# Kernel optimization log

Measured on AMD Instinct MI355X. Metric: run time of the kernel, lower is better.

The kernel has to match this reference:

```python
import jax, jax.numpy as jnp
import numpy as np

MARGIN = 0.1
SEMIHARD = True


def setup_inputs() -> dict:
    key = jax.random.key(0)
    k1, k2 = jax.random.split(key)
    N, D = 512, 128
    embeddings = jax.random.normal(k1, (N, D), dtype=jnp.float32)
    labels = jax.random.randint(k2, (N,), 0, 64, dtype=jnp.int64)
    return {"embeddings": embeddings, "labels": labels}


def _triplet_mask(labels):
    # mask[a, p, n] True iff a,p,n distinct, labels[a]==labels[p], labels[a]!=labels[n]
    n = labels.shape[0]
    ine = ~jnp.eye(n, dtype=bool)                       # [N, N] i != j
    distinct = ine[:, :, None] & ine[:, None, :] & ine[None, :, :]
    leq = labels[None, :] == labels[:, None]            # [N, N] label equality
    valid = leq[:, :, None] & ~leq[:, None, :]
    return distinct & valid


def reference(embeddings, labels):
    # L2-normalize rows, cosine similarity matrix
    norms = jnp.linalg.norm(embeddings, ord=2, axis=1, keepdims=True)
    e = embeddings / norms
    all_sim = e @ e.T                                   # [N, N]
    mask = _triplet_mask(labels).astype(all_sim.dtype)  # [N, N, N]
    # loss[a,p,n] = relu(-sim[a,p] + sim[a,n] + margin) * mask
    anc_pos = all_sim[:, :, None]                       # [N, N, 1]
    anc_neg = all_sim[:, None, :]                       # [N, 1, N]
    loss = jax.nn.relu(anc_neg - anc_pos + MARGIN) * mask
    if SEMIHARD:
        num_active = jnp.sum((loss > 1e-16).astype(loss.dtype))
        return jnp.sum(loss) / (num_active + 1e-16)
    else:
        return jnp.sum(loss) / jnp.sum(mask)
```

## Files before the change

kernel.cpp:

```cpp
#include <hip/hip_runtime.h>
#include <math.h>

#define MARGIN 0.1f
#define NN 512
#define DD 128
#define NT 512
#define AB 2
#define GROUPS (NT / 4)
#define NTILES (NN / GROUPS)
#define NBLK (NN / AB)
#define MAXPOS 256

__global__ __launch_bounds__(NT) void triplet_partial_kernel(
        const float* __restrict__ emb, const int* __restrict__ labels,
        double* __restrict__ part_sum, int* __restrict__ part_cnt) {
    __shared__ int   lab[NN];
    __shared__ __align__(16) float ea[AB][DD];
    __shared__ float simr[AB][NN];
    __shared__ int   pos[AB][MAXPOS];
    __shared__ int   npos[AB];
    __shared__ double red_s[NT / 64];
    __shared__ int    red_c[NT / 64];

    const int b  = blockIdx.x;
    const int t  = threadIdx.x;
    const int a0 = b * AB;
    const int g  = t >> 2;
    const int ks = t & 3;

    lab[t] = labels[t];
    if (t < AB * DD) {
        ea[t >> 7][t & 127] = emb[(size_t)(a0 + (t >> 7)) * DD + (t & 127)];
    }
    if (t < AB) npos[t] = 0;
    __syncthreads();

    const float4* __restrict__ emb4 = reinterpret_cast<const float4*>(emb);
    const float4* ea4 = reinterpret_cast<const float4*>(&ea[0][0]);

    float4 w0[8], w1[8];
    #pragma unroll
    for (int i2 = 0; i2 < 8; ++i2) {
        w0[i2] = ea4[i2 * 4 + ks];
        w1[i2] = ea4[32 + i2 * 4 + ks];
    }

    float nsq0 = 0.f, nsq1 = 0.f;
    #pragma unroll
    for (int i2 = 0; i2 < 8; ++i2) {
        nsq0 += w0[i2].x * w0[i2].x + w0[i2].y * w0[i2].y
              + w0[i2].z * w0[i2].z + w0[i2].w * w0[i2].w;
        nsq1 += w1[i2].x * w1[i2].x + w1[i2].y * w1[i2].y
              + w1[i2].z * w1[i2].z + w1[i2].w * w1[i2].w;
    }
    nsq0 += __shfl_xor(nsq0, 1, 64); nsq0 += __shfl_xor(nsq0, 2, 64);
    nsq1 += __shfl_xor(nsq1, 1, 64); nsq1 += __shfl_xor(nsq1, 2, 64);
    const float inva0 = 1.0f / sqrtf(nsq0);
    const float inva1 = 1.0f / sqrtf(nsq1);

    #pragma unroll 2
    for (int tl = 0; tl < NTILES; ++tl) {
        const int r = tl * GROUPS + g;
        float4 v[8];
        #pragma unroll
        for (int i2 = 0; i2 < 8; ++i2)
            v[i2] = emb4[(size_t)r * 32 + i2 * 4 + ks];

        float d0a = 0.f, d0b = 0.f, d1a = 0.f, d1b = 0.f, na = 0.f, nb = 0.f;
        #pragma unroll
        for (int i2 = 0; i2 < 8; i2 += 2) {
            d0a += v[i2].x * w0[i2].x + v[i2].y * w0[i2].y
                 + v[i2].z * w0[i2].z + v[i2].w * w0[i2].w;
            d1a += v[i2].x * w1[i2].x + v[i2].y * w1[i2].y
                 + v[i2].z * w1[i2].z + v[i2].w * w1[i2].w;
            na  += v[i2].x * v[i2].x + v[i2].y * v[i2].y
                 + v[i2].z * v[i2].z + v[i2].w * v[i2].w;
            const int j2 = i2 + 1;
            d0b += v[j2].x * w0[j2].x + v[j2].y * w0[j2].y
                 + v[j2].z * w0[j2].z + v[j2].w * w0[j2].w;
            d1b += v[j2].x * w1[j2].x + v[j2].y * w1[j2].y
                 + v[j2].z * w1[j2].z + v[j2].w * w1[j2].w;
            nb  += v[j2].x * v[j2].x + v[j2].y * v[j2].y
                 + v[j2].z * v[j2].z + v[j2].w * v[j2].w;
        }
        float d0 = d0a + d0b, d1 = d1a + d1b, nsq = na + nb;

        d0  += __shfl_xor(d0, 1, 64);  d0  += __shfl_xor(d0, 2, 64);
        d1  += __shfl_xor(d1, 1, 64);  d1  += __shfl_xor(d1, 2, 64);
        nsq += __shfl_xor(nsq, 1, 64); nsq += __shfl_xor(nsq, 2, 64);
        if (ks == 0) {
            const float rn = 1.0f / sqrtf(nsq);
            simr[0][r] = d0 * inva0 * rn;
            simr[1][r] = d1 * inva1 * rn;
        }
    }
    __syncthreads();

    {
        const int j = t;
        #pragma unroll
        for (int ai = 0; ai < AB; ++ai) {
            if (j != a0 + ai && lab[j] == lab[a0 + ai]) {
                int idx = atomicAdd(&npos[ai], 1);
                if (idx < MAXPOS) pos[ai][idx] = j;
            }
        }
    }
    __syncthreads();

    const int   myLab = lab[t];
    const float sn0   = simr[0][t];
    const float sn1   = simr[1][t];
    double lsum = 0.0;
    int    lcnt = 0;
    {
        const int la = lab[a0];
        if (myLab != la) {
            const int np = min(npos[0], MAXPOS);
            for (int pi = 0; pi < np; ++pi) {
                const float sap = simr[0][pos[0][pi]];
                const float d = sn0 - sap + MARGIN;
                if (d > 0.f)    lsum += (double)d;
                if (d > 1e-16f) lcnt += 1;
            }
        }
    }
    {
        const int la = lab[a0 + 1];
        if (myLab != la) {
            const int np = min(npos[1], MAXPOS);
            for (int pi = 0; pi < np; ++pi) {
                const float sap = simr[1][pos[1][pi]];
                const float d = sn1 - sap + MARGIN;
                if (d > 0.f)    lsum += (double)d;
                if (d > 1e-16f) lcnt += 1;
            }
        }
    }

    for (int off = 32; off > 0; off >>= 1) {
        lsum += __shfl_down(lsum, off, 64);
        lcnt += __shfl_down(lcnt, off, 64);
    }
    const int wid = t >> 6, lane = t & 63;
    if (lane == 0) { red_s[wid] = lsum; red_c[wid] = lcnt; }
    __syncthreads();
    if (t == 0) {
        double s = 0.0; int c = 0;
        for (int w = 0; w < NT / 64; ++w) { s += red_s[w]; c += red_c[w]; }
        part_sum[b] = s;
        part_cnt[b] = c;
    }
}

__global__ __launch_bounds__(NBLK) void finalize_kernel(
        const double* __restrict__ part_sum, const int* __restrict__ part_cnt,
        float* __restrict__ out) {
    __shared__ double rs[NBLK / 64];
    __shared__ int    rc[NBLK / 64];
    const int t = threadIdx.x;
    double s = part_sum[t];
    int    c = part_cnt[t];
    for (int off = 32; off > 0; off >>= 1) {
        s += __shfl_down(s, off, 64);
        c += __shfl_down(c, off, 64);
    }
    const int wid = t >> 6, lane = t & 63;
    if (lane == 0) { rs[wid] = s; rc[wid] = c; }
    __syncthreads();
    if (t == 0) {
        double S = 0.0; int C = 0;
        for (int w = 0; w < NBLK / 64; ++w) { S += rs[w]; C += rc[w]; }
        out[0] = (float)(S / ((double)C + 1e-16));
    }
}

extern "C" void kernel_launch(void* const* d_in, const int* in_sizes, int n_in,
                              void* d_out, int out_size, void* d_ws, size_t ws_size,
                              hipStream_t stream) {
    const float* emb  = (const float*)d_in[0];
    const int* labels = (const int*)d_in[1];

    double* part_sum = (double*)d_ws;
    int*    part_cnt = (int*)((char*)d_ws + NBLK * sizeof(double));
    float*  out      = (float*)d_out;

    triplet_partial_kernel<<<NBLK, NT, 0, stream>>>(emb, labels, part_sum, part_cnt);
    finalize_kernel<<<1, NBLK, 0, stream>>>(part_sum, part_cnt, out);
}
```

Baseline: 63.29 us.

## Fuse final reduction into main kernel via last-block atomic counters

After: 66.49 us. 1.05x slower.

```diff
diff --git a/kernel.cpp b/kernel.cpp
--- a/kernel.cpp
+++ b/kernel.cpp
@@ -6,19 +6,23 @@
 #define DD 128
 #define NT 512
 #define AB 2
+#define NBLK (NN / AB)
 #define GROUPS (NT / 4)
 #define NTILES (NN / GROUPS)
-#define NBLK (NN / AB)
 #define MAXPOS 256
-
-__global__ __launch_bounds__(NT) void triplet_partial_kernel(
+#define NSUB 8
+#define GSZ (NBLK / NSUB)
+
+__global__ __launch_bounds__(NT) void triplet_fused_kernel(
         const float* __restrict__ emb, const int* __restrict__ labels,
-        double* __restrict__ part_sum, int* __restrict__ part_cnt) {
+        double* __restrict__ part_sum, int* __restrict__ part_cnt,
+        unsigned* __restrict__ sub_cnt, unsigned* __restrict__ super_cnt,
+        const unsigned* __restrict__ probe, float* __restrict__ out) {
     __shared__ int   lab[NN];
-    __shared__ __align__(16) float ea[AB][DD];
     __shared__ float simr[AB][NN];
     __shared__ int   pos[AB][MAXPOS];
     __shared__ int   npos[AB];
+    __shared__ int   islast;
     __shared__ double red_s[NT / 64];
     __shared__ int    red_c[NT / 64];
 
@@ -29,20 +33,15 @@
     const int ks = t & 3;
 
     lab[t] = labels[t];
-    if (t < AB * DD) {
-        ea[t >> 7][t & 127] = emb[(size_t)(a0 + (t >> 7)) * DD + (t & 127)];
-    }
     if (t < AB) npos[t] = 0;
-    __syncthreads();
 
     const float4* __restrict__ emb4 = reinterpret_cast<const float4*>(emb);
-    const float4* ea4 = reinterpret_cast<const float4*>(&ea[0][0]);
 
     float4 w0[8], w1[8];
     #pragma unroll
     for (int i2 = 0; i2 < 8; ++i2) {
-        w0[i2] = ea4[i2 * 4 + ks];
-        w1[i2] = ea4[32 + i2 * 4 + ks];
+        w0[i2] = emb4[(size_t)a0 * 32 + i2 * 4 + ks];
+        w1[i2] = emb4[(size_t)(a0 + 1) * 32 + i2 * 4 + ks];
     }
 
     float nsq0 = 0.f, nsq1 = 0.f;
@@ -57,6 +56,16 @@
     nsq1 += __shfl_xor(nsq1, 1, 64); nsq1 += __shfl_xor(nsq1, 2, 64);
     const float inva0 = 1.0f / sqrtf(nsq0);
     const float inva1 = 1.0f / sqrtf(nsq1);
+
+    __syncthreads();
+
+    #pragma unroll
+    for (int ai = 0; ai < AB; ++ai) {
+        if (t != a0 + ai && lab[t] == lab[a0 + ai]) {
+            int idx = atomicAdd(&npos[ai], 1);
+            if (idx < MAXPOS) pos[ai][idx] = t;
+        }
+    }
 
     #pragma unroll 2
     for (int tl = 0; tl < NTILES; ++tl) {
@@ -96,30 +105,17 @@
     }
     __syncthreads();
 
-    {
-        const int j = t;
-        #pragma unroll
-        for (int ai = 0; ai < AB; ++ai) {
-            if (j != a0 + ai && lab[j] == lab[a0 + ai]) {
-                int idx = atomicAdd(&npos[ai], 1);
-                if (idx < MAXPOS) pos[ai][idx] = j;
-            }
-        }
-    }
-    __syncthreads();
-
     const int   myLab = lab[t];
-    const float sn0   = simr[0][t];
-    const float sn1   = simr[1][t];
     double lsum = 0.0;
     int    lcnt = 0;
     {
         const int la = lab[a0];
         if (myLab != la) {
+            const float sn = simr[0][t];
             const int np = min(npos[0], MAXPOS);
             for (int pi = 0; pi < np; ++pi) {
                 const float sap = simr[0][pos[0][pi]];
-                const float d = sn0 - sap + MARGIN;
+                const float d = sn - sap + MARGIN;
                 if (d > 0.f)    lsum += (double)d;
                 if (d > 1e-16f) lcnt += 1;
             }
@@ -128,10 +124,11 @@
     {
         const int la = lab[a0 + 1];
         if (myLab != la) {
+            const float sn = simr[1][t];
             const int np = min(npos[1], MAXPOS);
             for (int pi = 0; pi < np; ++pi) {
                 const float sap = simr[1][pos[1][pi]];
-                const float d = sn1 - sap + MARGIN;
+                const float d = sn - sap + MARGIN;
                 if (d > 0.f)    lsum += (double)d;
                 if (d > 1e-16f) lcnt += 1;
             }
@@ -147,31 +144,48 @@
     __syncthreads();
     if (t == 0) {
         double s = 0.0; int c = 0;
-        for (int w = 0; w < NT / 64; ++w) { s += red_s[w]; c += red_c[w]; }
-        part_sum[b] = s;
-        part_cnt[b] = c;
-    }
-}
-
-__global__ __launch_bounds__(NBLK) void finalize_kernel(
-        const double* __restrict__ part_sum, const int* __restrict__ part_cnt,
-        float* __restrict__ out) {
-    __shared__ double rs[NBLK / 64];
-    __shared__ int    rc[NBLK / 64];
-    const int t = threadIdx.x;
-    double s = part_sum[t];
-    int    c = part_cnt[t];
-    for (int off = 32; off > 0; off >>= 1) {
-        s += __shfl_down(s, off, 64);
-        c += __shfl_down(c, off, 64);
-    }
-    const int wid = t >> 6, lane = t & 63;
-    if (lane == 0) { rs[wid] = s; rc[wid] = c; }
-    __syncthreads();
-    if (t == 0) {
-        double S = 0.0; int C = 0;
-        for (int w = 0; w < NBLK / 64; ++w) { S += rs[w]; C += rc[w]; }
-        out[0] = (float)(S / ((double)C + 1e-16));
+        for (int w2 = 0; w2 < NT / 64; ++w2) { s += red_s[w2]; c += red_c[w2]; }
+        __hip_atomic_store(&part_sum[b], s, __ATOMIC_RELAXED,
+                           __HIP_MEMORY_SCOPE_AGENT);
+        __hip_atomic_store(&part_cnt[b], c, __ATOMIC_RELAXED,
+                           __HIP_MEMORY_SCOPE_AGENT);
+        const unsigned P = __hip_atomic_load(probe, __ATOMIC_RELAXED,
+                                             __HIP_MEMORY_SCOPE_AGENT);
+        unsigned old = __hip_atomic_fetch_add(&sub_cnt[(b & (NSUB - 1)) * 16],
+                                              1u, __ATOMIC_ACQ_REL,
+                                              __HIP_MEMORY_SCOPE_AGENT);
+        int win = 0;
+        if (((old - P + 1u) & (unsigned)(GSZ - 1)) == 0u) {
+            unsigned old2 = __hip_atomic_fetch_add(super_cnt, 1u,
+                                                   __ATOMIC_ACQ_REL,
+                                                   __HIP_MEMORY_SCOPE_AGENT);
+            win = (((old2 - P + 1u) & (unsigned)(NSUB - 1)) == 0u);
+        }
+        islast = win;
+    }
+    __syncthreads();
+
+    if (islast) {
+        double s = 0.0; int c = 0;
+        if (t < NBLK) {
+            s = __hip_atomic_load(&part_sum[t], __ATOMIC_RELAXED,
+                                  __HIP_MEMORY_SCOPE_AGENT);
+            c = __hip_atomic_load(&part_cnt[t], __ATOMIC_RELAXED,
+                                  __HIP_MEMORY_SCOPE_AGENT);
+        }
+        for (int off = 32; off > 0; off >>= 1) {
+            s += __shfl_down(s, off, 64);
+            c += __shfl_down(c, off, 64);
+        }
+        if (lane == 0) { red_s[wid] = s; red_c[wid] = c; }
+        __syncthreads();
+        if (t == 0) {
+            double S = 0.0; int C = 0;
+            for (int w2 = 0; w2 < NT / 64; ++w2) { S += red_s[w2]; C += red_c[w2]; }
+            float r = (float)(S / ((double)C + 1e-16));
+            __hip_atomic_store(out, r, __ATOMIC_RELEASE,
+                               __HIP_MEMORY_SCOPE_AGENT);
+        }
     }
 }
 
@@ -181,10 +195,15 @@
     const float* emb  = (const float*)d_in[0];
     const int* labels = (const int*)d_in[1];
 
-    double* part_sum = (double*)d_ws;
-    int*    part_cnt = (int*)((char*)d_ws + NBLK * sizeof(double));
-    float*  out      = (float*)d_out;
-
-    triplet_partial_kernel<<<NBLK, NT, 0, stream>>>(emb, labels, part_sum, part_cnt);
-    finalize_kernel<<<1, NBLK, 0, stream>>>(part_sum, part_cnt, out);
+    char* ws = (char*)d_ws;
+    double*   part_sum  = (double*)ws;
+    int*      part_cnt  = (int*)(ws + 2048);
+    unsigned* sub_cnt   = (unsigned*)(ws + 4096);
+    unsigned* super_cnt = (unsigned*)(ws + 4608);
+    const unsigned* probe = (const unsigned*)(ws + 8192);
+    float*    out       = (float*)d_out;
+
+    triplet_fused_kernel<<<NBLK, NT, 0, stream>>>(emb, labels, part_sum,
+                                                  part_cnt, sub_cnt, super_cnt,
+                                                  probe, out);
 }
```

## Fuse finalize reduction into main kernel via per-block flags

Applied to the files above, without the earlier changes.

Measured after the change: 65.09 us. 2.8% more time.

```diff
diff --git a/kernel.cpp b/kernel.cpp
--- a/kernel.cpp
+++ b/kernel.cpp
@@ -6,14 +6,17 @@
 #define DD 128
 #define NT 512
 #define AB 2
+#define NBLK (NN / AB)
 #define GROUPS (NT / 4)
 #define NTILES (NN / GROUPS)
-#define NBLK (NN / AB)
 #define MAXPOS 256
-
-__global__ __launch_bounds__(NT) void triplet_partial_kernel(
+#define FLAGVAL(P) ((P) ^ 0x5A5A5A5Au)
+
+__global__ __launch_bounds__(NT) void triplet_fused_kernel(
         const float* __restrict__ emb, const int* __restrict__ labels,
-        double* __restrict__ part_sum, int* __restrict__ part_cnt) {
+        double* __restrict__ part_sum, int* __restrict__ part_cnt,
+        unsigned* __restrict__ flags, const unsigned* __restrict__ probe,
+        float* __restrict__ out) {
     __shared__ int   lab[NN];
     __shared__ __align__(16) float ea[AB][DD];
     __shared__ float simr[AB][NN];
@@ -21,6 +24,8 @@
     __shared__ int   npos[AB];
     __shared__ double red_s[NT / 64];
     __shared__ int    red_c[NT / 64];
+    __shared__ double blk0_s;
+    __shared__ int    blk0_c;
 
     const int b  = blockIdx.x;
     const int t  = threadIdx.x;
@@ -147,31 +152,50 @@
     __syncthreads();
     if (t == 0) {
         double s = 0.0; int c = 0;
-        for (int w = 0; w < NT / 64; ++w) { s += red_s[w]; c += red_c[w]; }
-        part_sum[b] = s;
-        part_cnt[b] = c;
-    }
-}
-
-__global__ __launch_bounds__(NBLK) void finalize_kernel(
-        const double* __restrict__ part_sum, const int* __restrict__ part_cnt,
-        float* __restrict__ out) {
-    __shared__ double rs[NBLK / 64];
-    __shared__ int    rc[NBLK / 64];
-    const int t = threadIdx.x;
-    double s = part_sum[t];
-    int    c = part_cnt[t];
-    for (int off = 32; off > 0; off >>= 1) {
-        s += __shfl_down(s, off, 64);
-        c += __shfl_down(c, off, 64);
-    }
-    const int wid = t >> 6, lane = t & 63;
-    if (lane == 0) { rs[wid] = s; rc[wid] = c; }
-    __syncthreads();
-    if (t == 0) {
-        double S = 0.0; int C = 0;
-        for (int w = 0; w < NBLK / 64; ++w) { S += rs[w]; C += rc[w]; }
-        out[0] = (float)(S / ((double)C + 1e-16));
+        for (int w2 = 0; w2 < NT / 64; ++w2) { s += red_s[w2]; c += red_c[w2]; }
+        if (b != 0) {
+            __hip_atomic_store(&part_sum[b], s, __ATOMIC_RELAXED,
+                               __HIP_MEMORY_SCOPE_AGENT);
+            __hip_atomic_store(&part_cnt[b], c, __ATOMIC_RELAXED,
+                               __HIP_MEMORY_SCOPE_AGENT);
+            const unsigned P = __hip_atomic_load(probe, __ATOMIC_RELAXED,
+                                                 __HIP_MEMORY_SCOPE_AGENT);
+            __hip_atomic_store(&flags[(size_t)b * 16], FLAGVAL(P),
+                               __ATOMIC_RELEASE, __HIP_MEMORY_SCOPE_AGENT);
+        } else {
+            blk0_s = s; blk0_c = c;
+        }
+    }
+
+    if (b == 0) {
+        __syncthreads();
+        const unsigned P = __hip_atomic_load(probe, __ATOMIC_RELAXED,
+                                             __HIP_MEMORY_SCOPE_AGENT);
+        double s = 0.0; int c = 0;
+        if (t >= 1 && t < NBLK) {
+            while (__hip_atomic_load(&flags[(size_t)t * 16], __ATOMIC_ACQUIRE,
+                                     __HIP_MEMORY_SCOPE_AGENT) == P) {
+                __builtin_amdgcn_s_sleep(2);
+            }
+            s = __hip_atomic_load(&part_sum[t], __ATOMIC_RELAXED,
+                                  __HIP_MEMORY_SCOPE_AGENT);
+            c = __hip_atomic_load(&part_cnt[t], __ATOMIC_RELAXED,
+                                  __HIP_MEMORY_SCOPE_AGENT);
+        } else if (t == 0) {
+            s = blk0_s; c = blk0_c;
+        }
+        for (int off = 32; off > 0; off >>= 1) {
+            s += __shfl_down(s, off, 64);
+            c += __shfl_down(c, off, 64);
+        }
+        __syncthreads();
+        if (lane == 0) { red_s[wid] = s; red_c[wid] = c; }
+        __syncthreads();
+        if (t == 0) {
+            double S = 0.0; int C = 0;
+            for (int w2 = 0; w2 < NT / 64; ++w2) { S += red_s[w2]; C += red_c[w2]; }
+            out[0] = (float)(S / ((double)C + 1e-16));
+        }
     }
 }
 
@@ -181,10 +205,13 @@
     const float* emb  = (const float*)d_in[0];
     const int* labels = (const int*)d_in[1];
 
-    double* part_sum = (double*)d_ws;
-    int*    part_cnt = (int*)((char*)d_ws + NBLK * sizeof(double));
-    float*  out      = (float*)d_out;
-
-    triplet_partial_kernel<<<NBLK, NT, 0, stream>>>(emb, labels, part_sum, part_cnt);
-    finalize_kernel<<<1, NBLK, 0, stream>>>(part_sum, part_cnt, out);
+    char* ws = (char*)d_ws;
+    double*   part_sum = (double*)ws;
+    int*      part_cnt = (int*)(ws + 2048);
+    unsigned* flags    = (unsigned*)(ws + 4096);
+    const unsigned* probe = (const unsigned*)(ws + 65536);
+    float*    out      = (float*)d_out;
+
+    triplet_fused_kernel<<<NBLK, NT, 0, stream>>>(emb, labels, part_sum,
+                                                  part_cnt, flags, probe, out);
 }
```
